# Optimization experiments

Hardware: AMD Instinct MI355X
Metric: run time of the kernel (lower is better)

The kernel has to match this reference:

```python
import jax, jax.numpy as jnp
import numpy as np

B, L, E, H, V, T, NL = 32, 512, 512, 1024, 32000, 64, 2


def setup_inputs() -> dict:
    key = jax.random.key(0)
    ks = jax.random.split(key, 24)
    u = lambda k, s, a=0.05: jax.random.uniform(k, s, jnp.float32, -a, a)
    return {
        "enc_output": jax.random.normal(ks[0], (B, L, H), jnp.float32),
        "trg": jax.random.randint(ks[1], (B, T), 0, V, dtype=jnp.int64),
        "emb": u(ks[2], (V, E), 0.1),
        "W_att_enc": u(ks[3], (H, H)), "b_att_enc": jnp.zeros((H,), jnp.float32),
        "W_att_dec": u(ks[4], (H, H)), "b_att_dec": jnp.zeros((H,), jnp.float32),
        "v_att": u(ks[5], (H,)),
        "W_in": u(ks[6], (E, E + H)), "b_in": jnp.zeros((E,), jnp.float32),
        "W_ih0": u(ks[7], (4 * H, E)), "W_hh0": u(ks[8], (4 * H, H)),
        "b_ih0": jnp.zeros((4 * H,), jnp.float32), "b_hh0": jnp.zeros((4 * H,), jnp.float32),
        "W_ih1": u(ks[9], (4 * H, H)), "W_hh1": u(ks[10], (4 * H, H)),
        "b_ih1": jnp.zeros((4 * H,), jnp.float32), "b_hh1": jnp.zeros((4 * H,), jnp.float32),
        "W_fc": u(ks[11], (V, H), 0.1), "b_fc": jnp.zeros((V,), jnp.float32),
        "is_train": 0, "is_test": 1, "max_len": T, "sos_idx": 1,
    }


def _lstm_cell(x, h, c, W_ih, W_hh, b_ih, b_hh):
    g = x @ W_ih.T + b_ih + h @ W_hh.T + b_hh  # [B, 4H]
    i, f, gg, o = jnp.split(g, 4, axis=-1)     # torch gate order i,f,g,o
    c2 = jax.nn.sigmoid(f) * c + jax.nn.sigmoid(i) * jnp.tanh(gg)
    h2 = jax.nn.sigmoid(o) * jnp.tanh(c2)
    return h2, c2


def reference(enc_output, trg, emb, W_att_enc, b_att_enc, W_att_dec, b_att_dec,
              v_att, W_in, b_in, W_ih0, W_hh0, b_ih0, b_hh0, W_ih1, W_hh1,
              b_ih1, b_hh1, W_fc, b_fc, is_train, is_test, max_len, sos_idx):
    b = trg.shape[0]
    # precompute encoder projection for additive attention: [B, L, H]
    enc_proj = jnp.einsum('blh,ah->bla', enc_output, W_att_enc) + b_att_enc

    def step(carry, _):
        h, c, token = carry                    # h, c: [NL, B, H]
        emb_t = emb[token]                     # [B, E]
        q = h[-1] @ W_att_dec.T + b_att_dec    # [B, H]
        energy = jnp.tanh(enc_proj + q[:, None, :])
        alpha = jax.nn.softmax(energy @ v_att, axis=-1)        # [B, L]
        ctx = jnp.einsum('bl,blh->bh', alpha, enc_output)      # [B, H]
        x = jnp.concatenate([emb_t, ctx], axis=-1) @ W_in.T + b_in  # [B, E]
        h0, c0 = _lstm_cell(x, h[0], c[0], W_ih0, W_hh0, b_ih0, b_hh0)
        h1, c1 = _lstm_cell(h0, h[1], c[1], W_ih1, W_hh1, b_ih1, b_hh1)
        pred = h1 @ W_fc.T + b_fc              # [B, V]
        tok = jnp.argmax(pred, axis=1).astype(jnp.int32)
        return (jnp.stack([h0, h1]), jnp.stack([c0, c1]), tok), (pred, tok)

    h0 = jnp.zeros((NL, b, H), jnp.float32)
    init = (h0, h0, trg[:, 0].astype(jnp.int32))
    _, (preds, toks) = jax.lax.scan(step, init, None, length=max_len - 1)
    outputs = jnp.concatenate([jnp.zeros((1, b, V), preds.dtype), preds], 0)
    outputs = outputs.transpose(1, 0, 2)       # [B, max_len, V]
    _pred = jnp.concatenate(
        [jnp.full((b, 1), sos_idx, jnp.int32), toks.T], axis=1).astype(jnp.float32)
    return outputs, _pred
```

## Files before the change

### kernel.cpp

```cpp
#include <hip/hip_runtime.h>
#include <math.h>

#define BB 32
#define LL 512
#define EE 512
#define HH 1024
#define VV 32000
#define TT 64
#define G4 4096
#define NPRED 33024

__device__ __forceinline__ float fast_tanh(float x){
  float ax = fabsf(x);
  float e = __expf(ax + ax);
  float r = 1.0f - 2.0f/(e + 1.0f);
  return copysignf(r, x);
}

__global__ void k_init(float* __restrict__ outp, float* __restrict__ a0t,
                       float* __restrict__ a1t, float* __restrict__ c0,
                       float* __restrict__ c1, float* __restrict__ q,
                       const float* __restrict__ bad, int* __restrict__ token,
                       const int* __restrict__ trg, const int* __restrict__ sosp,
                       float* __restrict__ predout){
  int idx = blockIdx.x*256 + threadIdx.x;
  if (idx < 1024000){ int b = idx / VV; int v = idx % VV;
    outp[(size_t)b*TT*VV + v] = 0.f; return; }
  idx -= 1024000;
  if (idx < 49152){ a0t[idx]=0.f; return; } idx -= 49152;
  if (idx < 65536){ a1t[idx]=0.f; return; } idx -= 65536;
  if (idx < 32768){ c0[idx]=0.f; return; } idx -= 32768;
  if (idx < 32768){ c1[idx]=0.f; return; } idx -= 32768;
  if (idx < 32768){ q[idx] = bad[idx & (HH-1)]; return; } idx -= 32768;
  if (idx < 32){ token[idx] = trg[idx*TT]; return; } idx -= 32;
  if (idx < 32){ predout[idx*TT] = (float)(*sosp); return; }
}

__global__ void k_transpose(const float* __restrict__ src, int ss,
                            float* __restrict__ dst, int ds, int R, int C){
  __shared__ float tile[32][33];
  int c0 = blockIdx.x*32, r0 = blockIdx.y*32;
  int tx = threadIdx.x, ty = threadIdx.y;
  #pragma unroll
  for (int i=0;i<32;i+=8)
    tile[ty+i][tx] = src[(size_t)(r0+ty+i)*ss + c0+tx];
  __syncthreads();
  #pragma unroll
  for (int i=0;i<32;i+=8)
    dst[(size_t)(c0+ty+i)*ds + r0+tx] = tile[tx][ty+i];
}

__global__ __launch_bounds__(256) void k_pregemm(const float* __restrict__ AT,
    const float* __restrict__ WT, const float* __restrict__ bias,
    float* __restrict__ Cout, int N, int Kdim){
  int mt = blockIdx.x, ntg = blockIdx.y;
  int w = threadIdx.x >> 6, lane = threadIdx.x & 63;
  int m = mt*64 + lane;
  int nbase = ntg*128 + w*32;
  float acc[32];
  #pragma unroll
  for (int j=0;j<32;j++) acc[j]=0.f;
  const float* ap = AT + m;
  const float* wp = WT + nbase;
  for (int k=0;k<Kdim;k++){
    float a = ap[(size_t)k*16384];
    const float4* w4 = (const float4*)(wp + (size_t)k*N);
    #pragma unroll
    for (int j4=0;j4<8;j4++){
      float4 wv = w4[j4];
      acc[j4*4+0] = fmaf(a, wv.x, acc[j4*4+0]);
      acc[j4*4+1] = fmaf(a, wv.y, acc[j4*4+1]);
      acc[j4*4+2] = fmaf(a, wv.z, acc[j4*4+2]);
      acc[j4*4+3] = fmaf(a, wv.w, acc[j4*4+3]);
    }
  }
  __shared__ float tile[64][133];
  #pragma unroll
  for (int j=0;j<32;j++){
    float bv = bias ? bias[nbase+j] : 0.f;
    tile[lane][w*32+j] = acc[j] + bv;
  }
  __syncthreads();
  #pragma unroll
  for (int i=0;i<32;i++){
    int flat = i*256 + threadIdx.x;
    int mm = flat >> 7, nn = flat & 127;
    Cout[(size_t)(mt*64+mm)*N + ntg*128 + nn] = tile[mm][nn];
  }
}

__global__ __launch_bounds__(256) void k_scorepred(const float* __restrict__ ep,
    const float* __restrict__ partP, const float* __restrict__ bad,
    const float* __restrict__ vatt, float* __restrict__ scores,
    const float* __restrict__ b_fc, float* __restrict__ outp,
    float* __restrict__ argv, int* __restrict__ argi, int t){
  int vb = blockIdx.x;
  int w = threadIdx.x >> 6, lane = threadIdx.x & 63;
  if (vb < 512){
    int b = vb & 31, lt = vb >> 5;
    __shared__ float qs[HH], vs[HH];
    for (int i=threadIdx.x; i<HH; i+=256){
      float qv = bad[i];
      if (t > 1){
        qv += partP[(size_t)b*NPRED + VV + i]
            + partP[(size_t)(32+b)*NPRED + VV + i]
            + partP[(size_t)(64+b)*NPRED + VV + i]
            + partP[(size_t)(96+b)*NPRED + VV + i];
      }
      qs[i] = qv;
      vs[i] = vatt[i];
    }
    __syncthreads();
    #pragma unroll
    for (int i=0;i<8;i++){
      int l = lt*32 + w*8 + i;
      const float4* row = (const float4*)(ep + ((size_t)(b*LL + l))*HH);
      float acc = 0.f;
      #pragma unroll
      for (int c=0;c<4;c++){
        float4 xv = row[c*64 + lane];
        float4 qv = ((const float4*)qs)[c*64 + lane];
        float4 vv = ((const float4*)vs)[c*64 + lane];
        acc += fast_tanh(xv.x+qv.x)*vv.x;
        acc += fast_tanh(xv.y+qv.y)*vv.y;
        acc += fast_tanh(xv.z+qv.z)*vv.z;
        acc += fast_tanh(xv.w+qv.w)*vv.w;
      }
      #pragma unroll
      for (int d=32; d>0; d>>=1) acc += __shfl_down(acc, d);
      if (lane==0) scores[b*LL + l] = acc;
    }
  } else {
    if (t <= 1) return;
    int pb = vb - 512;
    int n = pb*256 + threadIdx.x;
    int tm1 = t - 1;
    float bias = b_fc[n];
    const float* p0 = partP + n;
    const float* p1 = partP + (size_t)32*NPRED + n;
    const float* p2 = partP + (size_t)64*NPRED + n;
    const float* p3 = partP + (size_t)96*NPRED + n;
    for (int b=0;b<32;b++){
      float v = p0[(size_t)b*NPRED] + p1[(size_t)b*NPRED]
              + p2[(size_t)b*NPRED] + p3[(size_t)b*NPRED] + bias;
      outp[(size_t)(b*TT + tm1)*VV + n] = v;
      float bv = v; int bi = n;
      #pragma unroll
      for (int d=32; d>0; d>>=1){
        float ov = __shfl_down(bv, d); int oi = __shfl_down(bi, d);
        if (ov > bv || (ov==bv && oi < bi)){ bv=ov; bi=oi; }
      }
      if (lane==0){
        argv[(pb*4 + w)*32 + b] = bv;
        argi[(pb*4 + w)*32 + b] = bi;
      }
    }
  }
}

__global__ __launch_bounds__(512) void k_attnx(const float* __restrict__ scores,
    const float* __restrict__ encW2, const float* __restrict__ emb,
    const int* __restrict__ token, const float* __restrict__ W1T,
    const float* __restrict__ b_in, float* __restrict__ A0T,
    const float* __restrict__ argv, const int* __restrict__ argi,
    float* __restrict__ predout, int t){
  int b = blockIdx.x, et = blockIdx.y;
  int tx = threadIdx.x;
  int w = tx >> 6, lane = tx & 63;
  __shared__ float alpha[LL];
  __shared__ float embs[EE];
  __shared__ float redm[8], reds[8];
  __shared__ float comb[8][64];
  __shared__ int tokS;
  if (t > 1){
    if (w==0){
      float bv = -INFINITY; int bi = 0x7fffffff;
      for (int j=lane; j<500; j+=64){
        float v = argv[j*32 + b]; int ix = argi[j*32 + b];
        if (v > bv || (v==bv && ix < bi)){ bv=v; bi=ix; }
      }
      #pragma unroll
      for (int d=32; d>0; d>>=1){
        float ov = __shfl_down(bv, d); int oi = __shfl_down(bi, d);
        if (ov > bv || (ov==bv && oi < bi)){ bv=ov; bi=oi; }
      }
      if (lane==0){
        tokS = bi;
        if (et==0) predout[b*TT + (t-1)] = (float)bi;
      }
    }
  } else if (tx==0) tokS = token[b];
  float s = scores[b*LL + tx];
  float mx = s;
  #pragma unroll
  for (int d=32; d>0; d>>=1) mx = fmaxf(mx, __shfl_down(mx, d));
  if (lane==0) redm[w] = mx;
  __syncthreads();
  mx = redm[0];
  #pragma unroll
  for (int i=1;i<8;i++) mx = fmaxf(mx, redm[i]);
  float e0 = __expf(s - mx);
  float sm = e0;
  #pragma unroll
  for (int d=32; d>0; d>>=1) sm += __shfl_down(sm, d);
  if (lane==0) reds[w] = sm;
  __syncthreads();
  sm = reds[0]+reds[1]+reds[2]+reds[3]+reds[4]+reds[5]+reds[6]+reds[7];
  alpha[tx] = e0 / sm;
  int tok = tokS;
  embs[tx] = emb[(size_t)tok*EE + tx];
  __syncthreads();
  int e = et*64 + lane;
  float acc = 0.f;
  const float* cw = encW2 + (size_t)b*LL*EE + (size_t)w*64*EE + e;
  #pragma unroll 4
  for (int l=0;l<64;l++) acc = fmaf(alpha[w*64+l], cw[(size_t)l*EE], acc);
  const float* wp = W1T + (size_t)w*64*EE + e;
  #pragma unroll 4
  for (int j=0;j<64;j++) acc = fmaf(embs[w*64+j], wp[(size_t)j*EE], acc);
  comb[w][lane] = acc;
  __syncthreads();
  if (w==0){
    float r = comb[0][lane]+comb[1][lane]+comb[2][lane]+comb[3][lane]
            + comb[4][lane]+comb[5][lane]+comb[6][lane]+comb[7][lane] + b_in[e];
    A0T[e*32 + b] = r;
  }
}

__device__ __forceinline__ void fma_step(float (&acc)[8][4], const float4 wv,
                                         const float4 a0, const float4 a1){
  acc[0][0]=fmaf(a0.x,wv.x,acc[0][0]); acc[0][1]=fmaf(a0.x,wv.y,acc[0][1]);
  acc[0][2]=fmaf(a0.x,wv.z,acc[0][2]); acc[0][3]=fmaf(a0.x,wv.w,acc[0][3]);
  acc[1][0]=fmaf(a0.y,wv.x,acc[1][0]); acc[1][1]=fmaf(a0.y,wv.y,acc[1][1]);
  acc[1][2]=fmaf(a0.y,wv.z,acc[1][2]); acc[1][3]=fmaf(a0.y,wv.w,acc[1][3]);
  acc[2][0]=fmaf(a0.z,wv.x,acc[2][0]); acc[2][1]=fmaf(a0.z,wv.y,acc[2][1]);
  acc[2][2]=fmaf(a0.z,wv.z,acc[2][2]); acc[2][3]=fmaf(a0.z,wv.w,acc[2][3]);
  acc[3][0]=fmaf(a0.w,wv.x,acc[3][0]); acc[3][1]=fmaf(a0.w,wv.y,acc[3][1]);
  acc[3][2]=fmaf(a0.w,wv.z,acc[3][2]); acc[3][3]=fmaf(a0.w,wv.w,acc[3][3]);
  acc[4][0]=fmaf(a1.x,wv.x,acc[4][0]); acc[4][1]=fmaf(a1.x,wv.y,acc[4][1]);
  acc[4][2]=fmaf(a1.x,wv.z,acc[4][2]); acc[4][3]=fmaf(a1.x,wv.w,acc[4][3]);
  acc[5][0]=fmaf(a1.y,wv.x,acc[5][0]); acc[5][1]=fmaf(a1.y,wv.y,acc[5][1]);
  acc[5][2]=fmaf(a1.y,wv.z,acc[5][2]); acc[5][3]=fmaf(a1.y,wv.w,acc[5][3]);
  acc[6][0]=fmaf(a1.z,wv.x,acc[6][0]); acc[6][1]=fmaf(a1.z,wv.y,acc[6][1]);
  acc[6][2]=fmaf(a1.z,wv.z,acc[6][2]); acc[6][3]=fmaf(a1.z,wv.w,acc[6][3]);
  acc[7][0]=fmaf(a1.w,wv.x,acc[7][0]); acc[7][1]=fmaf(a1.w,wv.y,acc[7][1]);
  acc[7][2]=fmaf(a1.w,wv.z,acc[7][2]); acc[7][3]=fmaf(a1.w,wv.w,acc[7][3]);
}

template<int KSLICE>
__global__ __launch_bounds__(256) void k_gemm2(const float* __restrict__ AT,
    const float* __restrict__ WT, float* __restrict__ partial, int N){
  __shared__ __align__(16) float As[KSLICE*32];
  int nt = blockIdx.x, ks = blockIdx.y;
  int w = threadIdx.x >> 6, lane = threadIdx.x & 63;
  int k0 = ks*KSLICE;
  const float4* asrc = (const float4*)(AT + (size_t)k0*32);
  for (int i=threadIdx.x; i<KSLICE*8; i+=256)
    ((float4*)As)[i] = asrc[i];
  __syncthreads();
  int n0 = nt*256 + lane*4;
  int b0 = w*8;
  float acc[8][4];
  #pragma unroll
  for (int i=0;i<8;i++)
    #pragma unroll
    for (int j=0;j<4;j++) acc[i][j]=0.f;
  const float* wp = WT + (size_t)k0*N + n0;
  const float* ap = As + b0;
  float4 w0 = *(const float4*)(wp);
  float4 w1 = *(const float4*)(wp + (size_t)N);
  float4 w2 = *(const float4*)(wp + (size_t)2*N);
  float4 w3 = *(const float4*)(wp + (size_t)3*N);
  wp += (size_t)4*N;
#define GSTEP(WREG) { float4 a0 = *(const float4*)(ap); \
                      float4 a1 = *(const float4*)(ap+4); ap += 32; \
                      fma_step(acc, WREG, a0, a1); }
  for (int k=0; k<KSLICE-4; k+=4){
    float4 p0 = *(const float4*)(wp);
    float4 p1 = *(const float4*)(wp + (size_t)N);
    float4 p2 = *(const float4*)(wp + (size_t)2*N);
    float4 p3 = *(const float4*)(wp + (size_t)3*N);
    wp += (size_t)4*N;
    GSTEP(w0); GSTEP(w1); GSTEP(w2); GSTEP(w3);
    w0 = p0; w1 = p1; w2 = p2; w3 = p3;
  }
  GSTEP(w0); GSTEP(w1); GSTEP(w2); GSTEP(w3);
#undef GSTEP
  float* pp = partial + ((size_t)ks*32 + b0)*N + n0;
  #pragma unroll
  for (int bi=0;bi<8;bi++)
    *(float4*)(pp + (size_t)bi*N) =
      make_float4(acc[bi][0],acc[bi][1],acc[bi][2],acc[bi][3]);
}

__global__ __launch_bounds__(128) void k_cell(const float* __restrict__ partial,
    const float* __restrict__ b_ih, const float* __restrict__ b_hh,
    float* __restrict__ c, float* __restrict__ hdst1, float* __restrict__ hdst2){
  int idx = blockIdx.x*128 + threadIdx.x;
  int b = idx >> 10, h = idx & 1023;
  const float* pb = partial + (size_t)b*G4;
  float gi = b_ih[h]      + b_hh[h];
  float gf = b_ih[1024+h] + b_hh[1024+h];
  float gg = b_ih[2048+h] + b_hh[2048+h];
  float go = b_ih[3072+h] + b_hh[3072+h];
  #pragma unroll 8
  for (int ks=0; ks<32; ks++){
    const float* pp = pb + (size_t)ks*32*G4;
    gi += pp[h]; gf += pp[1024+h]; gg += pp[2048+h]; go += pp[3072+h];
  }
  float cv = c[idx];
  float si = 1.f/(1.f+expf(-gi));
  float sf = 1.f/(1.f+expf(-gf));
  float so = 1.f/(1.f+expf(-go));
  float tg = tanhf(gg);
  float c2 = sf*cv + si*tg;
  float h2 = so*tanhf(c2);
  c[idx] = c2;
  hdst1[h*32 + b] = h2;
  if (hdst2) hdst2[h*32 + b] = h2;
}

__global__ __launch_bounds__(256) void k_predsum(const float* __restrict__ partP,
    const float* __restrict__ b_fc, float* __restrict__ outp,
    float* __restrict__ argv, int* __restrict__ argi, int t){
  int n = blockIdx.x*256 + threadIdx.x;
  int w = threadIdx.x >> 6, lane = threadIdx.x & 63;
  float bias = b_fc[n];
  const float* p0 = partP + n;
  const float* p1 = partP + (size_t)32*NPRED + n;
  const float* p2 = partP + (size_t)64*NPRED + n;
  const float* p3 = partP + (size_t)96*NPRED + n;
  for (int b=0;b<32;b++){
    float v = p0[(size_t)b*NPRED] + p1[(size_t)b*NPRED]
            + p2[(size_t)b*NPRED] + p3[(size_t)b*NPRED] + bias;
    outp[(size_t)(b*TT + t)*VV + n] = v;
    float bv = v; int bi = n;
    #pragma unroll
    for (int d=32; d>0; d>>=1){
      float ov = __shfl_down(bv, d); int oi = __shfl_down(bi, d);
      if (ov > bv || (ov==bv && oi < bi)){ bv=ov; bi=oi; }
    }
    if (lane==0){
      argv[(blockIdx.x*4 + w)*32 + b] = bv;
      argi[(blockIdx.x*4 + w)*32 + b] = bi;
    }
  }
}

__global__ void k_argfinal(const float* __restrict__ argv,
                           const int* __restrict__ argi,
                           float* __restrict__ predout){
  int b = threadIdx.x >> 3, j = threadIdx.x & 7;
  float bv = -INFINITY; int bi = 0x7fffffff;
  for (int p=j; p<500; p+=8){
    float v = argv[p*32+b]; int ix = argi[p*32+b];
    if (v>bv || (v==bv && ix<bi)){ bv=v; bi=ix; }
  }
  #pragma unroll
  for (int d=4; d>0; d>>=1){
    float ov = __shfl_down(bv, d); int oi = __shfl_down(bi, d);
    if (ov>bv || (ov==bv && oi<bi)){ bv=ov; bi=oi; }
  }
  if (j==0) predout[b*TT + 63] = (float)bi;
}

extern "C" void kernel_launch(void* const* d_in, const int* in_sizes, int n_in,
                              void* d_out, int out_size, void* d_ws, size_t ws_size,
                              hipStream_t stream){
  const float* enc_output=(const float*)d_in[0];
  const int*   trg       =(const int*)d_in[1];
  const float* emb       =(const float*)d_in[2];
  const float* W_att_enc =(const float*)d_in[3];
  const float* b_att_enc =(const float*)d_in[4];
  const float* W_att_dec =(const float*)d_in[5];
  const float* b_att_dec =(const float*)d_in[6];
  const float* v_att     =(const float*)d_in[7];
  const float* W_in      =(const float*)d_in[8];
  const float* b_in      =(const float*)d_in[9];
  const float* W_ih0     =(const float*)d_in[10];
  const float* W_hh0     =(const float*)d_in[11];
  const float* b_ih0     =(const float*)d_in[12];
  const float* b_hh0     =(const float*)d_in[13];
  const float* W_ih1     =(const float*)d_in[14];
  const float* W_hh1     =(const float*)d_in[15];
  const float* b_ih1     =(const float*)d_in[16];
  const float* b_hh1     =(const float*)d_in[17];
  const float* W_fc      =(const float*)d_in[18];
  const float* b_fc      =(const float*)d_in[19];
  const int*   sosp      =(const int*)d_in[23];

  float* out = (float*)d_out;
  float* predout = out + (size_t)BB*TT*VV;
  float* ws = (float*)d_ws;

  float* WcatPT = ws;
  float* Wcat0T = ws + 33816576;
  float* Wcat1T = ws + 40108032;
  float* W1T    = ws + 48496640;
  float* WinCtxT= ws + 48758784;
  float* WattET = ws + 49283072;
  float* encT   = ws + 50331648;
  float* partP  = encT;
  float* ep     = ws + 67108864;
  float* encW2  = ws + 83886080;
  float* partLS = ws + 92274688;
  float* A0T    = ws + 96468992;
  float* A1T    = ws + 96518144;
  float* c0     = ws + 96583680;
  float* c1     = ws + 96616448;
  float* q      = ws + 96649216;
  float* scores = ws + 96681984;
  float* argv   = ws + 96698368;
  int*   argi   = (int*)(ws + 96714368);
  int*   token  = (int*)(ws + 96730368);

  k_init<<<dim3(4833), dim3(256), 0, stream>>>(out, A0T, A1T, c0, c1, q,
      b_att_dec, token, trg, sosp, predout);

  auto TR=[&](const float* src,int ss,float* dst,int ds,int R,int C){
    k_transpose<<<dim3(C/32, R/32), dim3(32,8), 0, stream>>>(src, ss, dst, ds, R, C);
  };
  TR(W_fc, 1024, WcatPT, NPRED, VV, 1024);
  TR(W_att_dec, 1024, WcatPT + VV, NPRED, 1024, 1024);
  TR(W_ih0, 512, Wcat0T, G4, G4, 512);
  TR(W_hh0, 1024, Wcat0T + (size_t)512*G4, G4, G4, 1024);
  TR(W_ih1, 1024, Wcat1T, G4, G4, 1024);
  TR(W_hh1, 1024, Wcat1T + (size_t)1024*G4, G4, G4, 1024);
  TR(W_in, 1536, W1T, 512, 512, 512);
  TR(W_in + 512, 1536, WinCtxT, 512, 512, 1024);
  TR(W_att_enc, 1024, WattET, 1024, 1024, 1024);
  TR(enc_output, 1024, encT, 16384, 16384, 1024);

  k_pregemm<<<dim3(256,8), dim3(256), 0, stream>>>(encT, WattET, b_att_enc, ep, 1024, 1024);
  k_pregemm<<<dim3(256,4), dim3(256), 0, stream>>>(encT, WinCtxT, nullptr, encW2, 512, 1024);

  for (int t=1; t<TT; t++){
    k_scorepred<<<dim3(637), dim3(256), 0, stream>>>(ep, partP, b_att_dec, v_att,
        scores, b_fc, out, argv, argi, t);
    k_attnx<<<dim3(32,8), dim3(512), 0, stream>>>(scores, encW2, emb, token,
        W1T, b_in, A0T, argv, argi, predout, t);
    k_gemm2<48><<<dim3(16,32), dim3(256), 0, stream>>>(A0T, Wcat0T, partLS, G4);
    k_cell<<<dim3(256), dim3(128), 0, stream>>>(partLS, b_ih0, b_hh0, c0,
        A0T + (size_t)512*32, A1T);
    k_gemm2<64><<<dim3(16,32), dim3(256), 0, stream>>>(A1T, Wcat1T, partLS, G4);
    k_cell<<<dim3(256), dim3(128), 0, stream>>>(partLS, b_ih1, b_hh1, c1,
        A1T + (size_t)1024*32, nullptr);
    k_gemm2<256><<<dim3(129,4), dim3(256), 0, stream>>>(A1T + (size_t)1024*32,
        WcatPT, partP, NPRED);
  }
  k_predsum<<<dim3(125), dim3(256), 0, stream>>>(partP, b_fc, out, argv, argi, 63);
  k_argfinal<<<dim3(1), dim3(256), 0, stream>>>(argv, argi, predout);
}
```

Baseline: 13.06 ms.

## Deepen prefetch in vocab GEMM, widen pregemm tile, split score blocks finer

Adds a k_gemm2w8 variant that prefetches eight weight rows per iteration instead of four, and uses it for the large output-projection GEMM. The aim is more memory-level parallelism on the weight stream that dominates each step. k_pregemm now computes two 64-row M tiles per block, so each weight load is reused twice, with half as many blocks launched. k_scorepred uses twice as many score blocks, each covering half as many rows, to improve occupancy, and k_attnx loops are unrolled further. The costs are higher register pressure and shared-memory staging done twice in pregemm.

```diff
diff --git a/kernel.cpp b/kernel.cpp
--- a/kernel.cpp
+++ b/kernel.cpp
@@ -55,37 +55,55 @@
     float* __restrict__ Cout, int N, int Kdim){
   int mt = blockIdx.x, ntg = blockIdx.y;
   int w = threadIdx.x >> 6, lane = threadIdx.x & 63;
-  int m = mt*64 + lane;
+  int m0 = mt*128 + lane;
   int nbase = ntg*128 + w*32;
-  float acc[32];
-  #pragma unroll
-  for (int j=0;j<32;j++) acc[j]=0.f;
-  const float* ap = AT + m;
+  float acc0[32], acc1[32];
+  #pragma unroll
+  for (int j=0;j<32;j++){ acc0[j]=0.f; acc1[j]=0.f; }
+  const float* ap = AT + m0;
   const float* wp = WT + nbase;
   for (int k=0;k<Kdim;k++){
-    float a = ap[(size_t)k*16384];
+    float a0 = ap[(size_t)k*16384];
+    float a1 = ap[(size_t)k*16384 + 64];
     const float4* w4 = (const float4*)(wp + (size_t)k*N);
     #pragma unroll
     for (int j4=0;j4<8;j4++){
       float4 wv = w4[j4];
-      acc[j4*4+0] = fmaf(a, wv.x, acc[j4*4+0]);
-      acc[j4*4+1] = fmaf(a, wv.y, acc[j4*4+1]);
-      acc[j4*4+2] = fmaf(a, wv.z, acc[j4*4+2]);
-      acc[j4*4+3] = fmaf(a, wv.w, acc[j4*4+3]);
+      acc0[j4*4+0] = fmaf(a0, wv.x, acc0[j4*4+0]);
+      acc0[j4*4+1] = fmaf(a0, wv.y, acc0[j4*4+1]);
+      acc0[j4*4+2] = fmaf(a0, wv.z, acc0[j4*4+2]);
+      acc0[j4*4+3] = fmaf(a0, wv.w, acc0[j4*4+3]);
+      acc1[j4*4+0] = fmaf(a1, wv.x, acc1[j4*4+0]);
+      acc1[j4*4+1] = fmaf(a1, wv.y, acc1[j4*4+1]);
+      acc1[j4*4+2] = fmaf(a1, wv.z, acc1[j4*4+2]);
+      acc1[j4*4+3] = fmaf(a1, wv.w, acc1[j4*4+3]);
     }
   }
   __shared__ float tile[64][133];
   #pragma unroll
   for (int j=0;j<32;j++){
     float bv = bias ? bias[nbase+j] : 0.f;
-    tile[lane][w*32+j] = acc[j] + bv;
+    tile[lane][w*32+j] = acc0[j] + bv;
   }
   __syncthreads();
   #pragma unroll
   for (int i=0;i<32;i++){
     int flat = i*256 + threadIdx.x;
     int mm = flat >> 7, nn = flat & 127;
-    Cout[(size_t)(mt*64+mm)*N + ntg*128 + nn] = tile[mm][nn];
+    Cout[(size_t)(mt*128+mm)*N + ntg*128 + nn] = tile[mm][nn];
+  }
+  __syncthreads();
+  #pragma unroll
+  for (int j=0;j<32;j++){
+    float bv = bias ? bias[nbase+j] : 0.f;
+    tile[lane][w*32+j] = acc1[j] + bv;
+  }
+  __syncthreads();
+  #pragma unroll
+  for (int i=0;i<32;i++){
+    int flat = i*256 + threadIdx.x;
+    int mm = flat >> 7, nn = flat & 127;
+    Cout[(size_t)(mt*128+64+mm)*N + ntg*128 + nn] = tile[mm][nn];
   }
 }
 
@@ -96,7 +114,7 @@
     float* __restrict__ argv, int* __restrict__ argi, int t){
   int vb = blockIdx.x;
   int w = threadIdx.x >> 6, lane = threadIdx.x & 63;
-  if (vb < 512){
+  if (vb < 1024){
     int b = vb & 31, lt = vb >> 5;
     __shared__ float qs[HH], vs[HH];
     for (int i=threadIdx.x; i<HH; i+=256){
@@ -112,8 +130,8 @@
     }
     __syncthreads();
     #pragma unroll
-    for (int i=0;i<8;i++){
-      int l = lt*32 + w*8 + i;
+    for (int i=0;i<4;i++){
+      int l = lt*16 + w*4 + i;
       const float4* row = (const float4*)(ep + ((size_t)(b*LL + l))*HH);
       float acc = 0.f;
       #pragma unroll
@@ -132,7 +150,7 @@
     }
   } else {
     if (t <= 1) return;
-    int pb = vb - 512;
+    int pb = vb - 1024;
     int n = pb*256 + threadIdx.x;
     int tm1 = t - 1;
     float bias = b_fc[n];
@@ -213,10 +231,10 @@
   int e = et*64 + lane;
   float acc = 0.f;
   const float* cw = encW2 + (size_t)b*LL*EE + (size_t)w*64*EE + e;
-  #pragma unroll 4
+  #pragma unroll 8
   for (int l=0;l<64;l++) acc = fmaf(alpha[w*64+l], cw[(size_t)l*EE], acc);
   const float* wp = W1T + (size_t)w*64*EE + e;
-  #pragma unroll 4
+  #pragma unroll 8
   for (int j=0;j<64;j++) acc = fmaf(embs[w*64+j], wp[(size_t)j*EE], acc);
   comb[w][lane] = acc;
   __syncthreads();
@@ -285,6 +303,62 @@
     w0 = p0; w1 = p1; w2 = p2; w3 = p3;
   }
   GSTEP(w0); GSTEP(w1); GSTEP(w2); GSTEP(w3);
+#undef GSTEP
+  float* pp = partial + ((size_t)ks*32 + b0)*N + n0;
+  #pragma unroll
+  for (int bi=0;bi<8;bi++)
+    *(float4*)(pp + (size_t)bi*N) =
+      make_float4(acc[bi][0],acc[bi][1],acc[bi][2],acc[bi][3]);
+}
+
+template<int KSLICE>
+__global__ __launch_bounds__(256) void k_gemm2w8(const float* __restrict__ AT,
+    const float* __restrict__ WT, float* __restrict__ partial, int N){
+  __shared__ __align__(16) float As[KSLICE*32];
+  int nt = blockIdx.x, ks = blockIdx.y;
+  int w = threadIdx.x >> 6, lane = threadIdx.x & 63;
+  int k0 = ks*KSLICE;
+  const float4* asrc = (const float4*)(AT + (size_t)k0*32);
+  for (int i=threadIdx.x; i<KSLICE*8; i+=256)
+    ((float4*)As)[i] = asrc[i];
+  __syncthreads();
+  int n0 = nt*256 + lane*4;
+  int b0 = w*8;
+  float acc[8][4];
+  #pragma unroll
+  for (int i=0;i<8;i++)
+    #pragma unroll
+    for (int j=0;j<4;j++) acc[i][j]=0.f;
+  const float* wp = WT + (size_t)k0*N + n0;
+  const float* ap = As + b0;
+  float4 w0 = *(const float4*)(wp);
+  float4 w1 = *(const float4*)(wp + (size_t)N);
+  float4 w2 = *(const float4*)(wp + (size_t)2*N);
+  float4 w3 = *(const float4*)(wp + (size_t)3*N);
+  float4 w4 = *(const float4*)(wp + (size_t)4*N);
+  float4 w5 = *(const float4*)(wp + (size_t)5*N);
+  float4 w6 = *(const float4*)(wp + (size_t)6*N);
+  float4 w7 = *(const float4*)(wp + (size_t)7*N);
+  wp += (size_t)8*N;
+#define GSTEP(WREG) { float4 a0 = *(const float4*)(ap); \
+                      float4 a1 = *(const float4*)(ap+4); ap += 32; \
+                      fma_step(acc, WREG, a0, a1); }
+  for (int k=0; k<KSLICE-8; k+=8){
+    float4 p0 = *(const float4*)(wp);
+    float4 p1 = *(const float4*)(wp + (size_t)N);
+    float4 p2 = *(const float4*)(wp + (size_t)2*N);
+    float4 p3 = *(const float4*)(wp + (size_t)3*N);
+    float4 p4 = *(const float4*)(wp + (size_t)4*N);
+    float4 p5 = *(const float4*)(wp + (size_t)5*N);
+    float4 p6 = *(const float4*)(wp + (size_t)6*N);
+    float4 p7 = *(const float4*)(wp + (size_t)7*N);
+    wp += (size_t)8*N;
+    GSTEP(w0); GSTEP(w1); GSTEP(w2); GSTEP(w3);
+    GSTEP(w4); GSTEP(w5); GSTEP(w6); GSTEP(w7);
+    w0=p0; w1=p1; w2=p2; w3=p3; w4=p4; w5=p5; w6=p6; w7=p7;
+  }
+  GSTEP(w0); GSTEP(w1); GSTEP(w2); GSTEP(w3);
+  GSTEP(w4); GSTEP(w5); GSTEP(w6); GSTEP(w7);
 #undef GSTEP
   float* pp = partial + ((size_t)ks*32 + b0)*N + n0;
   #pragma unroll
@@ -431,11 +505,11 @@
   TR(W_att_enc, 1024, WattET, 1024, 1024, 1024);
   TR(enc_output, 1024, encT, 16384, 16384, 1024);
 
-  k_pregemm<<<dim3(256,8), dim3(256), 0, stream>>>(encT, WattET, b_att_enc, ep, 1024, 1024);
-  k_pregemm<<<dim3(256,4), dim3(256), 0, stream>>>(encT, WinCtxT, nullptr, encW2, 512, 1024);
+  k_pregemm<<<dim3(128,8), dim3(256), 0, stream>>>(encT, WattET, b_att_enc, ep, 1024, 1024);
+  k_pregemm<<<dim3(128,4), dim3(256), 0, stream>>>(encT, WinCtxT, nullptr, encW2, 512, 1024);
 
   for (int t=1; t<TT; t++){
-    k_scorepred<<<dim3(637), dim3(256), 0, stream>>>(ep, partP, b_att_dec, v_att,
+    k_scorepred<<<dim3(1149), dim3(256), 0, stream>>>(ep, partP, b_att_dec, v_att,
         scores, b_fc, out, argv, argi, t);
     k_attnx<<<dim3(32,8), dim3(512), 0, stream>>>(scores, encW2, emb, token,
         W1T, b_in, A0T, argv, argi, predout, t);
@@ -445,7 +519,7 @@
     k_gemm2<64><<<dim3(16,32), dim3(256), 0, stream>>>(A1T, Wcat1T, partLS, G4);
     k_cell<<<dim3(256), dim3(128), 0, stream>>>(partLS, b_ih1, b_hh1, c1,
         A1T + (size_t)1024*32, nullptr);
-    k_gemm2<256><<<dim3(129,4), dim3(256), 0, stream>>>(A1T + (size_t)1024*32,
+    k_gemm2w8<256><<<dim3(129,4), dim3(256), 0, stream>>>(A1T + (size_t)1024*32,
         WcatPT, partP, NPRED);
   }
   k_predsum<<<dim3(125), dim3(256), 0, stream>>>(partP, b_fc, out, argv, argi, 63);
```

After: 11.67 ms. 1.12x faster.
